# Optimization experiments

Measured on AMD Instinct MI355X. Metric: run time of the kernel, lower is better.

Reference implementation:

```python
import jax, jax.numpy as jnp
import numpy as np

EPS = 1e-6

def setup_inputs() -> dict:
    key = jax.random.key(0)
    k1, k2, k3 = jax.random.split(key, 3)
    D = 1024
    return {
        "x": jax.random.normal(k1, (2, 2048, D), dtype=jnp.float32),
        "w_norm": jnp.ones((D,), dtype=jnp.float32),
        "w_qkv": jax.random.normal(k2, (3 * D, D), dtype=jnp.float32) * (1.0 / np.sqrt(D)),
        "w_out": jax.random.normal(k3, (D, D), dtype=jnp.float32) * (1.0 / np.sqrt(D)),
        "window_size": 128,
        "n_heads": 16,
    }

def reference(x, w_norm, w_qkv, w_out, window_size, n_heads):
    B, L, D = x.shape
    H = n_heads
    dh = D // H
    skip = x
    # RMSNorm
    rms = jnp.sqrt(jnp.mean(x * x, axis=-1, keepdims=True) + EPS)
    xn = w_norm * (x / rms)
    # QKV projection (torch Linear: y = x @ W.T)
    qkv = xn @ w_qkv.T  # [B, L, 3D]
    q, k, v = jnp.split(qkv, 3, axis=-1)
    q = q.reshape(B, L, H, dh).transpose(0, 2, 1, 3)  # [B,H,L,dh]
    k = k.reshape(B, L, H, dh).transpose(0, 2, 1, 3)
    v = v.reshape(B, L, H, dh).transpose(0, 2, 1, 3)
    scores = jnp.einsum("bhid,bhjd->bhij", q, k) / np.sqrt(dh)  # [B,H,L,L]
    # Symmetric window: token i attends to j in [i - w//2, i + w//2]
    idx = jnp.arange(L)
    half = window_size // 2
    band = jnp.abs(idx[:, None] - idx[None, :]) <= half  # [L, L]
    scores = jnp.where(band, scores, -jnp.inf)
    attn = jax.nn.softmax(scores, axis=-1)  # zeros outside band, matches torch loop
    out = jnp.einsum("bhij,bhjd->bhid", attn, v)  # [B,H,L,dh]
    out = out.transpose(0, 2, 1, 3).reshape(B, L, D)
    out = out @ w_out.T
    return out + skip
```

## Files before the change

kernel.cpp:

```cpp
#include <hip/hip_runtime.h>
#include <hip/hip_bf16.h>
#include <cstdint>

typedef float f32x4 __attribute__((ext_vector_type(4)));
typedef short s16x8 __attribute__((ext_vector_type(8)));
typedef short s16x4 __attribute__((ext_vector_type(4)));

constexpr int B_ = 2, L_ = 2048, D_ = 1024, H_ = 16, DH = 64, HALF = 64;
constexpr int M_ROWS = B_ * L_;
constexpr int QKV_N = 3 * D_;

__device__ __forceinline__ void gload16(const void* g, void* l) {
    __builtin_amdgcn_global_load_lds(
        (const __attribute__((address_space(1))) unsigned int*)g,
        (__attribute__((address_space(3))) unsigned int*)l, 16, 0, 0);
}

__device__ __forceinline__ void cfence() {
    __builtin_amdgcn_sched_barrier(0);
    asm volatile("" ::: "memory");
}

__global__ __launch_bounds__(256) void rmsnorm_kernel(const float* __restrict__ x,
                                                      const float* __restrict__ wn,
                                                      __hip_bfloat16* __restrict__ xn) {
    int w = threadIdx.x >> 6, lane = threadIdx.x & 63;
    int row = blockIdx.x * 4 + w;
    const float4* xr = reinterpret_cast<const float4*>(x + (size_t)row * D_);
    const float4* wr = reinterpret_cast<const float4*>(wn);
    float4 v[4];
    float ss = 0.f;
#pragma unroll
    for (int c = 0; c < 4; ++c) {
        v[c] = xr[c * 64 + lane];
        ss += v[c].x * v[c].x + v[c].y * v[c].y + v[c].z * v[c].z + v[c].w * v[c].w;
    }
#pragma unroll
    for (int off = 32; off; off >>= 1) ss += __shfl_xor(ss, off);
    float rinv = rsqrtf(ss * (1.0f / D_) + 1e-6f);
#pragma unroll
    for (int c = 0; c < 4; ++c) {
        float4 wv = wr[c * 64 + lane];
        s16x4 pk;
        float vals[4] = {v[c].x * rinv * wv.x, v[c].y * rinv * wv.y,
                         v[c].z * rinv * wv.z, v[c].w * rinv * wv.w};
#pragma unroll
        for (int e = 0; e < 4; ++e) {
            __hip_bfloat16 t = __float2bfloat16(vals[e]);
            pk[e] = *reinterpret_cast<short*>(&t);
        }
        *(s16x4*)(xn + (size_t)row * D_ + (c * 64 + lane) * 4) = pk;
    }
}

__global__ void cvt_weights_kernel(const float* __restrict__ wq, const float* __restrict__ wo,
                                   __hip_bfloat16* __restrict__ oq, __hip_bfloat16* __restrict__ oo) {
    constexpr int NQ4 = QKV_N * D_ / 4;
    int i = blockIdx.x * blockDim.x + threadIdx.x;
    const float* src; __hip_bfloat16* dst; int j;
    if (i < NQ4) { src = wq; dst = oq; j = i; }
    else         { src = wo; dst = oo; j = i - NQ4; }
    float4 v = reinterpret_cast<const float4*>(src)[j];
    s16x4 pk;
    float vals[4] = {v.x, v.y, v.z, v.w};
#pragma unroll
    for (int e = 0; e < 4; ++e) {
        __hip_bfloat16 t = __float2bfloat16(vals[e]);
        pk[e] = *reinterpret_cast<short*>(&t);
    }
    *(s16x4*)(dst + (size_t)j * 4) = pk;
}

template <int EPI, int BN>
__global__ __launch_bounds__(256, 2) void gemm_pipe_kernel(const __hip_bfloat16* __restrict__ A,
                                                           const __hip_bfloat16* __restrict__ Bt,
                                                           __hip_bfloat16* __restrict__ Cbf,
                                                           __hip_bfloat16* __restrict__ vT,
                                                           float* __restrict__ Cf,
                                                           const float* __restrict__ resid,
                                                           int M, int N, int K) {
    constexpr int BM = 128;
    constexpr int NFR = BN / 32;
    constexpr int ABYTES = BM * 128;
    constexpr int BBYTES = BN * 128;
    constexpr int BUF = ABYTES + BBYTES;
    constexpr int AISS = BM / 32, BISS = BN / 32, NISS = AISS + BISS;
    __shared__ __align__(16) char smem[2 * BUF];

    const int tid = threadIdx.x;
    const int lane = tid & 63;
    const int wid = tid >> 6;

    int nwg = gridDim.x * gridDim.y;
    int lin = blockIdx.y * gridDim.x + blockIdx.x;
    int cpx = nwg >> 3;
    int swz = (lin & 7) * cpx + (lin >> 3);
    int bx = swz % gridDim.x;
    int by = swz / gridDim.x;

    const int rowBase = by * BM;
    const int colBase = bx * BN;
    const int NTILES = K >> 6;

    const int srow = tid >> 3;
    const int colSw = ((tid & 7) ^ (srow & 7)) << 3;
    const __hip_bfloat16* aG = A + (size_t)(rowBase + srow) * K + colSw;
    const __hip_bfloat16* bG = Bt + (size_t)(colBase + srow) * K + colSw;
    const int dstW = wid << 10;

    const int wm = wid >> 1, wn = wid & 1;
    const int l15 = lane & 15, hi = lane >> 4;
    const int s7 = l15 & 7;
    const int rA = wm * 64 + l15;
    const int rB = wn * (BN / 2) + l15;

    f32x4 acc[4][NFR];
#pragma unroll
    for (int m = 0; m < 4; ++m)
#pragma unroll
        for (int n = 0; n < NFR; ++n) acc[m][n] = (f32x4){0.f, 0.f, 0.f, 0.f};

#pragma unroll
    for (int i = 0; i < AISS; ++i) gload16(aG + (size_t)(i * 32) * K, smem + i * 4096 + dstW);
#pragma unroll
    for (int i = 0; i < BISS; ++i) gload16(bG + (size_t)(i * 32) * K, smem + ABYTES + i * 4096 + dstW);

    for (int kt = 0; kt < NTILES; ++kt) {
        const int bf = kt & 1;
        if (kt + 1 < NTILES) {
            char* base = smem + (bf ^ 1) * BUF;
            const __hip_bfloat16* as = aG + (size_t)(kt + 1) * 64;
            const __hip_bfloat16* bs = bG + (size_t)(kt + 1) * 64;
#pragma unroll
            for (int i = 0; i < AISS; ++i) gload16(as + (size_t)(i * 32) * K, base + i * 4096 + dstW);
#pragma unroll
            for (int i = 0; i < BISS; ++i) gload16(bs + (size_t)(i * 32) * K, base + ABYTES + i * 4096 + dstW);
            if constexpr (NISS == 8)
                asm volatile("s_waitcnt vmcnt(8)" ::: "memory");
            else
                asm volatile("s_waitcnt vmcnt(6)" ::: "memory");
        } else {
            asm volatile("s_waitcnt vmcnt(0)" ::: "memory");
        }
        __builtin_amdgcn_s_barrier();
        cfence();

        const char* ab = smem + bf * BUF;
        const char* bb = ab + ABYTES;
        s16x8 af[4][2], bfr[NFR][2];
#pragma unroll
        for (int mf = 0; mf < 4; ++mf)
#pragma unroll
            for (int kk = 0; kk < 2; ++kk)
                af[mf][kk] = *(const s16x8*)(ab + (rA + mf * 16) * 128 + (((kk * 4 + hi) ^ s7) << 4));
#pragma unroll
        for (int nf = 0; nf < NFR; ++nf)
#pragma unroll
            for (int kk = 0; kk < 2; ++kk)
                bfr[nf][kk] = *(const s16x8*)(bb + (rB + nf * 16) * 128 + (((kk * 4 + hi) ^ s7) << 4));

        __builtin_amdgcn_s_setprio(1);
#pragma unroll
        for (int kk = 0; kk < 2; ++kk)
#pragma unroll
            for (int mf = 0; mf < 4; ++mf)
#pragma unroll
                for (int nf = 0; nf < NFR; ++nf)
                    acc[mf][nf] = __builtin_amdgcn_mfma_f32_16x16x32_bf16(af[mf][kk], bfr[nf][kk],
                                                                          acc[mf][nf], 0, 0, 0);
        __builtin_amdgcn_s_setprio(0);

        asm volatile("s_waitcnt lgkmcnt(0)" ::: "memory");
        __builtin_amdgcn_s_barrier();
        cfence();
    }

    if constexpr (EPI == 0) {
        if (colBase < 2 * D_) {
#pragma unroll
            for (int mf = 0; mf < 4; ++mf)
#pragma unroll
                for (int nf = 0; nf < NFR; ++nf) {
                    int col = colBase + wn * (BN / 2) + nf * 16 + l15;
                    int row0 = rowBase + wm * 64 + mf * 16 + 4 * hi;
#pragma unroll
                    for (int r = 0; r < 4; ++r)
                        Cbf[(size_t)(row0 + r) * N + col] = __float2bfloat16(acc[mf][nf][r]);
                }
        } else {
            char* Ct = smem;
#pragma unroll
            for (int mf = 0; mf < 4; ++mf)
#pragma unroll
                for (int nf = 0; nf < NFR; ++nf) {
                    int cl = wn * (BN / 2) + nf * 16 + l15;
#pragma unroll
                    for (int r = 0; r < 4; ++r) {
                        int rl = wm * 64 + mf * 16 + 4 * hi + r;
                        __hip_bfloat16 t = __float2bfloat16(acc[mf][nf][r]);
                        *(short*)(Ct + cl * 272 + rl * 2) = *reinterpret_cast<short*>(&t);
                    }
                }
            __syncthreads();
            int cl = tid >> 1, half = tid & 1;
            int gcol = colBase + cl - 2 * D_;
            int hh = gcol >> 6, dd = gcol & 63;
            int bb2 = rowBase >> 11, i0 = rowBase & (L_ - 1);
            __hip_bfloat16* dstp = vT + ((size_t)(bb2 * H_ + hh) * DH + dd) * L_ + i0 + half * 64;
#pragma unroll
            for (int ch = 0; ch < 8; ++ch) {
                s16x8 vv = *(const s16x8*)(Ct + cl * 272 + half * 128 + ch * 16);
                *(s16x8*)(dstp + ch * 8) = vv;
            }
        }
    } else {
#pragma unroll
        for (int mf = 0; mf < 4; ++mf)
#pragma unroll
            for (int nf = 0; nf < NFR; ++nf) {
                int col = colBase + wn * (BN / 2) + nf * 16 + l15;
                int row0 = rowBase + wm * 64 + mf * 16 + 4 * hi;
#pragma unroll
                for (int r = 0; r < 4; ++r)
                    Cf[(size_t)(row0 + r) * N + col] = acc[mf][nf][r] + resid[(size_t)(row0 + r) * N + col];
            }
    }
}

__global__ __launch_bounds__(128) void attn_mfma_kernel(const __hip_bfloat16* __restrict__ qkv,
                                                        const __hip_bfloat16* __restrict__ vT,
                                                        __hip_bfloat16* __restrict__ attn) {
    __shared__ __align__(16) char smem[49152];
    constexpr int VOFF = 24576;
    int tid = threadIdx.x;
    int lane = tid & 63, w = tid >> 6;
    int tq = blockIdx.x, h = blockIdx.y, b = blockIdx.z;
    int q0 = tq * 64;
    int jg0 = q0 - HALF;
    const __hip_bfloat16* qkvb = qkv + (size_t)(b * L_) * QKV_N;
    const __hip_bfloat16* vTg = vT + (size_t)(b * H_ + h) * DH * L_;

    int l15 = lane & 15, hi = lane >> 4;

    s16x8 aq[2][2];
#pragma unroll
    for (int m = 0; m < 2; ++m)
#pragma unroll
        for (int kk = 0; kk < 2; ++kk)
            aq[m][kk] = *(const s16x8*)(qkvb + (size_t)(q0 + 32 * w + 16 * m + l15) * QKV_N
                                        + h * DH + kk * 32 + hi * 8);

#pragma unroll
    for (int it = 0; it < 12; ++it) {
        int ob = (it * 2 + w) << 10;
        int o = ob + lane * 16;
        int row = o >> 7;
        int c = ((o >> 4) & 7) ^ (row & 7);
        int jg = jg0 + row;
        int jc = jg < 0 ? 0 : (jg > L_ - 1 ? L_ - 1 : jg);
        gload16(qkvb + (size_t)jc * QKV_N + D_ + h * DH + c * 8, smem + ob);
    }
#pragma unroll
    for (int it = 0; it < 12; ++it) {
        int ob = (it * 2 + w) << 10;
        int o = ob + lane * 16;
        int d = o / 384;
        int rem = o - d * 384;
        int c = (rem >> 4) ^ (d & 7);
        int kb = jg0 + c * 8;
        int kc = kb < 0 ? 0 : (kb > L_ - 8 ? L_ - 8 : kb);
        gload16(vTg + (size_t)d * L_ + kc, smem + VOFF + ob);
    }
    asm volatile("s_waitcnt vmcnt(12)" ::: "memory");
    __builtin_amdgcn_s_barrier();
    cfence();

    f32x4 sc[2][10];
#pragma unroll
    for (int m = 0; m < 2; ++m)
#pragma unroll
        for (int kt = 0; kt < 10; ++kt) sc[m][kt] = (f32x4){0.f, 0.f, 0.f, 0.f};

#pragma unroll
    for (int kt = 0; kt < 10; ++kt) {
        int jl = 32 * w + 16 * kt + l15;
        s16x8 bk0 = *(const s16x8*)(smem + jl * 128 + ((hi ^ (jl & 7)) * 16));
        s16x8 bk1 = *(const s16x8*)(smem + jl * 128 + (((4 + hi) ^ (jl & 7)) * 16));
#pragma unroll
        for (int m = 0; m < 2; ++m) {
            sc[m][kt] = __builtin_amdgcn_mfma_f32_16x16x32_bf16(aq[m][0], bk0, sc[m][kt], 0, 0, 0);
            sc[m][kt] = __builtin_amdgcn_mfma_f32_16x16x32_bf16(aq[m][1], bk1, sc[m][kt], 0, 0, 0);
        }
    }

#pragma unroll
    for (int m = 0; m < 2; ++m) {
#pragma unroll
        for (int r = 0; r < 4; ++r) {
            int iloc = 32 * w + 16 * m + 4 * hi + r;
            float mx = -1e30f;
#pragma unroll
            for (int kt = 0; kt < 10; ++kt) {
                int jl = 32 * w + 16 * kt + l15;
                int jg = jg0 + jl;
                bool ok = (jl >= iloc) && (jl <= iloc + 2 * HALF) && (jg >= 0) && (jg < L_);
                float s = ok ? sc[m][kt][r] * 0.125f : -1e30f;
                sc[m][kt][r] = s;
                mx = fmaxf(mx, s);
            }
            mx = fmaxf(mx, __shfl_xor(mx, 1));
            mx = fmaxf(mx, __shfl_xor(mx, 2));
            mx = fmaxf(mx, __shfl_xor(mx, 4));
            mx = fmaxf(mx, __shfl_xor(mx, 8));
            float sum = 0.f;
#pragma unroll
            for (int kt = 0; kt < 10; ++kt) {
                float p = __expf(sc[m][kt][r] - mx);
                sc[m][kt][r] = p;
                sum += p;
            }
            sum += __shfl_xor(sum, 1);
            sum += __shfl_xor(sum, 2);
            sum += __shfl_xor(sum, 4);
            sum += __shfl_xor(sum, 8);
            float inv = 1.0f / sum;
#pragma unroll
            for (int kt = 0; kt < 10; ++kt) sc[m][kt][r] *= inv;
        }
    }

    __syncthreads();

    {
        __hip_bfloat16* Pw = (__hip_bfloat16*)(smem + w * 10752);
#pragma unroll
        for (int m = 0; m < 2; ++m)
#pragma unroll
            for (int kt = 0; kt < 10; ++kt)
#pragma unroll
                for (int r = 0; r < 4; ++r)
                    Pw[(16 * m + 4 * hi + r) * 168 + 16 * kt + l15] = __float2bfloat16(sc[m][kt][r]);
    }
    __syncthreads();

    f32x4 o[2][4];
#pragma unroll
    for (int m = 0; m < 2; ++m)
#pragma unroll
        for (int nt = 0; nt < 4; ++nt) o[m][nt] = (f32x4){0.f, 0.f, 0.f, 0.f};

#pragma unroll
    for (int kst = 0; kst < 5; ++kst) {
        s16x8 ap[2];
#pragma unroll
        for (int m = 0; m < 2; ++m)
            ap[m] = *(const s16x8*)(smem + w * 10752 + (16 * m + l15) * 336 + (32 * kst + 8 * hi) * 2);
#pragma unroll
        for (int nt = 0; nt < 4; ++nt) {
            int d = 16 * nt + l15;
            int c = 4 * w + 4 * kst + hi;
            s16x8 bv = *(const s16x8*)(smem + VOFF + d * 384 + ((c ^ (d & 7)) << 4));
#pragma unroll
            for (int m = 0; m < 2; ++m)
                o[m][nt] = __builtin_amdgcn_mfma_f32_16x16x32_bf16(ap[m], bv, o[m][nt], 0, 0, 0);
        }
    }

#pragma unroll
    for (int m = 0; m < 2; ++m)
#pragma unroll
        for (int nt = 0; nt < 4; ++nt)
#pragma unroll
            for (int r = 0; r < 4; ++r) {
                int rowg = q0 + 32 * w + 16 * m + 4 * hi + r;
                attn[(size_t)(b * L_ + rowg) * D_ + h * DH + 16 * nt + l15] =
                    __float2bfloat16(o[m][nt][r]);
            }
}

extern "C" void kernel_launch(void* const* d_in, const int* in_sizes, int n_in,
                              void* d_out, int out_size, void* d_ws, size_t ws_size,
                              hipStream_t stream) {
    const float* x      = (const float*)d_in[0];
    const float* w_norm = (const float*)d_in[1];
    const float* w_qkv  = (const float*)d_in[2];
    const float* w_out  = (const float*)d_in[3];

    char* ws = (char*)d_ws;
    __hip_bfloat16* xn   = (__hip_bfloat16*)(ws);
    __hip_bfloat16* wq   = (__hip_bfloat16*)(ws + (8u  << 20));
    __hip_bfloat16* wo   = (__hip_bfloat16*)(ws + (14u << 20));
    __hip_bfloat16* qkv  = (__hip_bfloat16*)(ws + (16u << 20));
    __hip_bfloat16* attn = (__hip_bfloat16*)(ws + (40u << 20));
    __hip_bfloat16* vT   = (__hip_bfloat16*)(ws + (48u << 20));
    float* out = (float*)d_out;

    {
        int n4 = (QKV_N * D_ + D_ * D_) / 4;
        cvt_weights_kernel<<<n4 / 256, 256, 0, stream>>>(w_qkv, w_out, wq, wo);
    }

    rmsnorm_kernel<<<M_ROWS / 4, 256, 0, stream>>>(x, w_norm, xn);

    gemm_pipe_kernel<0, 128><<<dim3(QKV_N / 128, M_ROWS / 128), 256, 0, stream>>>(
        xn, wq, qkv, vT, nullptr, nullptr, M_ROWS, QKV_N, D_);

    attn_mfma_kernel<<<dim3(L_ / 64, H_, B_), 128, 0, stream>>>(qkv, vT, attn);

    gemm_pipe_kernel<1, 64><<<dim3(D_ / 64, M_ROWS / 128), 256, 0, stream>>>(
        attn, wo, nullptr, nullptr, out, x, M_ROWS, D_, D_);
}
```

Before: 92.35 us.

## Rewrite windowed attention with 32x32 MFMA and register-resident softmax; merge prep kernels

The attention kernel is rewritten to compute transposed scores with 32x32x16 MFMA, loading K and V fragments straight from global memory instead of staging them in LDS. Softmax runs in registers with only cross-half shuffles. P is repacked to bf16 through permlane32_swap, so the LDS round trip and its barriers are gone, and normalization is deferred to the output. Separately, weight conversion and RMSNorm are merged into one launch to save a kernel launch. The risk is uncoalesced, redundant global loads of K/V per wave in exchange for occupancy and fewer syncs.

```diff
diff --git a/kernel.cpp b/kernel.cpp
--- a/kernel.cpp
+++ b/kernel.cpp
@@ -3,8 +3,11 @@
 #include <cstdint>
 
 typedef float f32x4 __attribute__((ext_vector_type(4)));
+typedef float f32x16 __attribute__((ext_vector_type(16)));
 typedef short s16x8 __attribute__((ext_vector_type(8)));
 typedef short s16x4 __attribute__((ext_vector_type(4)));
+typedef unsigned int u32x2 __attribute__((ext_vector_type(2)));
+typedef unsigned int u32x4 __attribute__((ext_vector_type(4)));
 
 constexpr int B_ = 2, L_ = 2048, D_ = 1024, H_ = 16, DH = 64, HALF = 64;
 constexpr int M_ROWS = B_ * L_;
@@ -21,54 +24,60 @@
     asm volatile("" ::: "memory");
 }
 
-__global__ __launch_bounds__(256) void rmsnorm_kernel(const float* __restrict__ x,
-                                                      const float* __restrict__ wn,
-                                                      __hip_bfloat16* __restrict__ xn) {
-    int w = threadIdx.x >> 6, lane = threadIdx.x & 63;
-    int row = blockIdx.x * 4 + w;
-    const float4* xr = reinterpret_cast<const float4*>(x + (size_t)row * D_);
-    const float4* wr = reinterpret_cast<const float4*>(wn);
-    float4 v[4];
-    float ss = 0.f;
-#pragma unroll
-    for (int c = 0; c < 4; ++c) {
-        v[c] = xr[c * 64 + lane];
-        ss += v[c].x * v[c].x + v[c].y * v[c].y + v[c].z * v[c].z + v[c].w * v[c].w;
-    }
-#pragma unroll
-    for (int off = 32; off; off >>= 1) ss += __shfl_xor(ss, off);
-    float rinv = rsqrtf(ss * (1.0f / D_) + 1e-6f);
-#pragma unroll
-    for (int c = 0; c < 4; ++c) {
-        float4 wv = wr[c * 64 + lane];
+__global__ __launch_bounds__(256) void prep_kernel(const float* __restrict__ x,
+                                                   const float* __restrict__ wn,
+                                                   const float* __restrict__ wq,
+                                                   const float* __restrict__ wo,
+                                                   __hip_bfloat16* __restrict__ xn,
+                                                   __hip_bfloat16* __restrict__ oq,
+                                                   __hip_bfloat16* __restrict__ oo) {
+    constexpr int NQ4 = QKV_N * D_ / 4;
+    constexpr int NCVT = NQ4 + D_ * D_ / 4;
+    constexpr int CVTBLK = NCVT / 256;
+    int bid = blockIdx.x;
+    if (bid < CVTBLK) {
+        int i = bid * 256 + threadIdx.x;
+        const float* src; __hip_bfloat16* dst; int j;
+        if (i < NQ4) { src = wq; dst = oq; j = i; }
+        else         { src = wo; dst = oo; j = i - NQ4; }
+        float4 v = reinterpret_cast<const float4*>(src)[j];
         s16x4 pk;
-        float vals[4] = {v[c].x * rinv * wv.x, v[c].y * rinv * wv.y,
-                         v[c].z * rinv * wv.z, v[c].w * rinv * wv.w};
+        float vals[4] = {v.x, v.y, v.z, v.w};
 #pragma unroll
         for (int e = 0; e < 4; ++e) {
             __hip_bfloat16 t = __float2bfloat16(vals[e]);
             pk[e] = *reinterpret_cast<short*>(&t);
         }
-        *(s16x4*)(xn + (size_t)row * D_ + (c * 64 + lane) * 4) = pk;
-    }
-}
-
-__global__ void cvt_weights_kernel(const float* __restrict__ wq, const float* __restrict__ wo,
-                                   __hip_bfloat16* __restrict__ oq, __hip_bfloat16* __restrict__ oo) {
-    constexpr int NQ4 = QKV_N * D_ / 4;
-    int i = blockIdx.x * blockDim.x + threadIdx.x;
-    const float* src; __hip_bfloat16* dst; int j;
-    if (i < NQ4) { src = wq; dst = oq; j = i; }
-    else         { src = wo; dst = oo; j = i - NQ4; }
-    float4 v = reinterpret_cast<const float4*>(src)[j];
-    s16x4 pk;
-    float vals[4] = {v.x, v.y, v.z, v.w};
-#pragma unroll
-    for (int e = 0; e < 4; ++e) {
-        __hip_bfloat16 t = __float2bfloat16(vals[e]);
-        pk[e] = *reinterpret_cast<short*>(&t);
-    }
-    *(s16x4*)(dst + (size_t)j * 4) = pk;
+        *(s16x4*)(dst + (size_t)j * 4) = pk;
+    } else {
+        int w = threadIdx.x >> 6, lane = threadIdx.x & 63;
+        int row = (bid - CVTBLK) * 4 + w;
+        const float4* xr = reinterpret_cast<const float4*>(x + (size_t)row * D_);
+        const float4* wr = reinterpret_cast<const float4*>(wn);
+        float4 v[4];
+        float ss = 0.f;
+#pragma unroll
+        for (int c = 0; c < 4; ++c) {
+            v[c] = xr[c * 64 + lane];
+            ss += v[c].x * v[c].x + v[c].y * v[c].y + v[c].z * v[c].z + v[c].w * v[c].w;
+        }
+#pragma unroll
+        for (int off = 32; off; off >>= 1) ss += __shfl_xor(ss, off);
+        float rinv = rsqrtf(ss * (1.0f / D_) + 1e-6f);
+#pragma unroll
+        for (int c = 0; c < 4; ++c) {
+            float4 wv = wr[c * 64 + lane];
+            s16x4 pk;
+            float vals[4] = {v[c].x * rinv * wv.x, v[c].y * rinv * wv.y,
+                             v[c].z * rinv * wv.z, v[c].w * rinv * wv.w};
+#pragma unroll
+            for (int e = 0; e < 4; ++e) {
+                __hip_bfloat16 t = __float2bfloat16(vals[e]);
+                pk[e] = *reinterpret_cast<short*>(&t);
+            }
+            *(s16x4*)(xn + (size_t)row * D_ + (c * 64 + lane) * 4) = pk;
+        }
+    }
 }
 
 template <int EPI, int BN>
@@ -227,155 +236,113 @@
     }
 }
 
-__global__ __launch_bounds__(128) void attn_mfma_kernel(const __hip_bfloat16* __restrict__ qkv,
-                                                        const __hip_bfloat16* __restrict__ vT,
-                                                        __hip_bfloat16* __restrict__ attn) {
-    __shared__ __align__(16) char smem[49152];
-    constexpr int VOFF = 24576;
+__global__ __launch_bounds__(128, 2) void attn_mfma_kernel(const __hip_bfloat16* __restrict__ qkv,
+                                                           const __hip_bfloat16* __restrict__ vT,
+                                                           __hip_bfloat16* __restrict__ attn) {
     int tid = threadIdx.x;
-    int lane = tid & 63, w = tid >> 6;
+    int w = tid >> 6;
+    int lane = tid & 63;
+    int l31 = lane & 31, hi1 = lane >> 5;
     int tq = blockIdx.x, h = blockIdx.y, b = blockIdx.z;
-    int q0 = tq * 64;
-    int jg0 = q0 - HALF;
+    int qbase = tq * 64 + 32 * w;
+    int kb = qbase - HALF;
+    int qg = qbase + l31;
     const __hip_bfloat16* qkvb = qkv + (size_t)(b * L_) * QKV_N;
     const __hip_bfloat16* vTg = vT + (size_t)(b * H_ + h) * DH * L_;
 
-    int l15 = lane & 15, hi = lane >> 4;
-
-    s16x8 aq[2][2];
-#pragma unroll
-    for (int m = 0; m < 2; ++m)
-#pragma unroll
-        for (int kk = 0; kk < 2; ++kk)
-            aq[m][kk] = *(const s16x8*)(qkvb + (size_t)(q0 + 32 * w + 16 * m + l15) * QKV_N
-                                        + h * DH + kk * 32 + hi * 8);
-
-#pragma unroll
-    for (int it = 0; it < 12; ++it) {
-        int ob = (it * 2 + w) << 10;
-        int o = ob + lane * 16;
-        int row = o >> 7;
-        int c = ((o >> 4) & 7) ^ (row & 7);
-        int jg = jg0 + row;
-        int jc = jg < 0 ? 0 : (jg > L_ - 1 ? L_ - 1 : jg);
-        gload16(qkvb + (size_t)jc * QKV_N + D_ + h * DH + c * 8, smem + ob);
-    }
-#pragma unroll
-    for (int it = 0; it < 12; ++it) {
-        int ob = (it * 2 + w) << 10;
-        int o = ob + lane * 16;
-        int d = o / 384;
-        int rem = o - d * 384;
-        int c = (rem >> 4) ^ (d & 7);
-        int kb = jg0 + c * 8;
-        int kc = kb < 0 ? 0 : (kb > L_ - 8 ? L_ - 8 : kb);
-        gload16(vTg + (size_t)d * L_ + kc, smem + VOFF + ob);
-    }
-    asm volatile("s_waitcnt vmcnt(12)" ::: "memory");
-    __builtin_amdgcn_s_barrier();
-    cfence();
-
-    f32x4 sc[2][10];
-#pragma unroll
-    for (int m = 0; m < 2; ++m)
-#pragma unroll
-        for (int kt = 0; kt < 10; ++kt) sc[m][kt] = (f32x4){0.f, 0.f, 0.f, 0.f};
-
-#pragma unroll
-    for (int kt = 0; kt < 10; ++kt) {
-        int jl = 32 * w + 16 * kt + l15;
-        s16x8 bk0 = *(const s16x8*)(smem + jl * 128 + ((hi ^ (jl & 7)) * 16));
-        s16x8 bk1 = *(const s16x8*)(smem + jl * 128 + (((4 + hi) ^ (jl & 7)) * 16));
-#pragma unroll
-        for (int m = 0; m < 2; ++m) {
-            sc[m][kt] = __builtin_amdgcn_mfma_f32_16x16x32_bf16(aq[m][0], bk0, sc[m][kt], 0, 0, 0);
-            sc[m][kt] = __builtin_amdgcn_mfma_f32_16x16x32_bf16(aq[m][1], bk1, sc[m][kt], 0, 0, 0);
-        }
-    }
-
-#pragma unroll
-    for (int m = 0; m < 2; ++m) {
-#pragma unroll
-        for (int r = 0; r < 4; ++r) {
-            int iloc = 32 * w + 16 * m + 4 * hi + r;
-            float mx = -1e30f;
-#pragma unroll
-            for (int kt = 0; kt < 10; ++kt) {
-                int jl = 32 * w + 16 * kt + l15;
-                int jg = jg0 + jl;
-                bool ok = (jl >= iloc) && (jl <= iloc + 2 * HALF) && (jg >= 0) && (jg < L_);
-                float s = ok ? sc[m][kt][r] * 0.125f : -1e30f;
-                sc[m][kt][r] = s;
-                mx = fmaxf(mx, s);
+    s16x8 qf[4];
+#pragma unroll
+    for (int kk = 0; kk < 4; ++kk)
+        qf[kk] = *(const s16x8*)(qkvb + (size_t)qg * QKV_N + h * DH + kk * 16 + hi1 * 8);
+
+    f32x16 T[5];
+#pragma unroll
+    for (int kt = 0; kt < 5; ++kt) T[kt] = (f32x16)(0.f);
+#pragma unroll
+    for (int kt = 0; kt < 5; ++kt) {
+        int keyg = kb + 32 * kt + l31;
+        int kc = keyg < 0 ? 0 : (keyg > L_ - 1 ? L_ - 1 : keyg);
+        const __hip_bfloat16* kp = qkvb + (size_t)kc * QKV_N + D_ + h * DH + hi1 * 8;
+#pragma unroll
+        for (int kk = 0; kk < 4; ++kk) {
+            s16x8 kf = *(const s16x8*)(kp + kk * 16);
+            T[kt] = __builtin_amdgcn_mfma_f32_32x32x16_bf16(kf, qf[kk], T[kt], 0, 0, 0);
+        }
+    }
+
+    float mx = -1e30f;
+#pragma unroll
+    for (int kt = 0; kt < 5; ++kt) {
+#pragma unroll
+        for (int r = 0; r < 16; ++r) {
+            int koff = (r & 3) + 8 * (r >> 2) + 4 * hi1;
+            int keyg = kb + 32 * kt + koff;
+            int del = keyg - qg;
+            bool ok = (del >= -HALF) && (del <= HALF) && (keyg >= 0) && (keyg < L_);
+            float t = ok ? T[kt][r] * 0.125f : -1e30f;
+            T[kt][r] = t;
+            mx = fmaxf(mx, t);
+        }
+    }
+    mx = fmaxf(mx, __shfl_xor(mx, 32));
+    float sum = 0.f;
+#pragma unroll
+    for (int kt = 0; kt < 5; ++kt) {
+#pragma unroll
+        for (int r = 0; r < 16; ++r) {
+            float p = __expf(T[kt][r] - mx);
+            T[kt][r] = p;
+            sum += p;
+        }
+    }
+    sum += __shfl_xor(sum, 32);
+    float inv = 1.0f / sum;
+
+    u32x4 pu[10];
+#pragma unroll
+    for (int kt = 0; kt < 5; ++kt) {
+#pragma unroll
+        for (int s = 0; s < 2; ++s) {
+            unsigned P0, P1, P2, P3;
+            asm("v_cvt_pk_bf16_f32 %0, %1, %2" : "=v"(P0) : "v"(T[kt][8 * s + 0]), "v"(T[kt][8 * s + 1]));
+            asm("v_cvt_pk_bf16_f32 %0, %1, %2" : "=v"(P1) : "v"(T[kt][8 * s + 2]), "v"(T[kt][8 * s + 3]));
+            asm("v_cvt_pk_bf16_f32 %0, %1, %2" : "=v"(P2) : "v"(T[kt][8 * s + 4]), "v"(T[kt][8 * s + 5]));
+            asm("v_cvt_pk_bf16_f32 %0, %1, %2" : "=v"(P3) : "v"(T[kt][8 * s + 6]), "v"(T[kt][8 * s + 7]));
+            u32x2 sA = __builtin_amdgcn_permlane32_swap(P0, P2, false, false);
+            u32x2 sB = __builtin_amdgcn_permlane32_swap(P1, P3, false, false);
+            pu[2 * kt + s] = (u32x4){sA[0], sB[0], sA[1], sB[1]};
+        }
+    }
+
+    f32x16 O[2];
+#pragma unroll
+    for (int dt = 0; dt < 2; ++dt) O[dt] = (f32x16)(0.f);
+#pragma unroll
+    for (int t = 0; t < 10; ++t) {
+        int kv = kb + 16 * t + 8 * hi1;
+        kv = kv < 0 ? 0 : (kv > L_ - 8 ? L_ - 8 : kv);
+        s16x8 pf = __builtin_bit_cast(s16x8, pu[t]);
+#pragma unroll
+        for (int dt = 0; dt < 2; ++dt) {
+            s16x8 vf = *(const s16x8*)(vTg + (size_t)(32 * dt + l31) * L_ + kv);
+            O[dt] = __builtin_amdgcn_mfma_f32_32x32x16_bf16(vf, pf, O[dt], 0, 0, 0);
+        }
+    }
+
+    __hip_bfloat16* ob = attn + (size_t)(b * L_ + qg) * D_ + h * DH;
+#pragma unroll
+    for (int dt = 0; dt < 2; ++dt) {
+#pragma unroll
+        for (int rr = 0; rr < 4; ++rr) {
+            s16x4 pk4;
+#pragma unroll
+            for (int j = 0; j < 4; ++j) {
+                __hip_bfloat16 tb = __float2bfloat16(O[dt][4 * rr + j] * inv);
+                pk4[j] = *reinterpret_cast<short*>(&tb);
             }
-            mx = fmaxf(mx, __shfl_xor(mx, 1));
-            mx = fmaxf(mx, __shfl_xor(mx, 2));
-            mx = fmaxf(mx, __shfl_xor(mx, 4));
-            mx = fmaxf(mx, __shfl_xor(mx, 8));
-            float sum = 0.f;
-#pragma unroll
-            for (int kt = 0; kt < 10; ++kt) {
-                float p = __expf(sc[m][kt][r] - mx);
-                sc[m][kt][r] = p;
-                sum += p;
-            }
-            sum += __shfl_xor(sum, 1);
-            sum += __shfl_xor(sum, 2);
-            sum += __shfl_xor(sum, 4);
-            sum += __shfl_xor(sum, 8);
-            float inv = 1.0f / sum;
-#pragma unroll
-            for (int kt = 0; kt < 10; ++kt) sc[m][kt][r] *= inv;
-        }
-    }
-
-    __syncthreads();
-
-    {
-        __hip_bfloat16* Pw = (__hip_bfloat16*)(smem + w * 10752);
-#pragma unroll
-        for (int m = 0; m < 2; ++m)
-#pragma unroll
-            for (int kt = 0; kt < 10; ++kt)
-#pragma unroll
-                for (int r = 0; r < 4; ++r)
-                    Pw[(16 * m + 4 * hi + r) * 168 + 16 * kt + l15] = __float2bfloat16(sc[m][kt][r]);
-    }
-    __syncthreads();
-
-    f32x4 o[2][4];
-#pragma unroll
-    for (int m = 0; m < 2; ++m)
-#pragma unroll
-        for (int nt = 0; nt < 4; ++nt) o[m][nt] = (f32x4){0.f, 0.f, 0.f, 0.f};
-
-#pragma unroll
-    for (int kst = 0; kst < 5; ++kst) {
-        s16x8 ap[2];
-#pragma unroll
-        for (int m = 0; m < 2; ++m)
-            ap[m] = *(const s16x8*)(smem + w * 10752 + (16 * m + l15) * 336 + (32 * kst + 8 * hi) * 2);
-#pragma unroll
-        for (int nt = 0; nt < 4; ++nt) {
-            int d = 16 * nt + l15;
-            int c = 4 * w + 4 * kst + hi;
-            s16x8 bv = *(const s16x8*)(smem + VOFF + d * 384 + ((c ^ (d & 7)) << 4));
-#pragma unroll
-            for (int m = 0; m < 2; ++m)
-                o[m][nt] = __builtin_amdgcn_mfma_f32_16x16x32_bf16(ap[m], bv, o[m][nt], 0, 0, 0);
-        }
-    }
-
-#pragma unroll
-    for (int m = 0; m < 2; ++m)
-#pragma unroll
-        for (int nt = 0; nt < 4; ++nt)
-#pragma unroll
-            for (int r = 0; r < 4; ++r) {
-                int rowg = q0 + 32 * w + 16 * m + 4 * hi + r;
-                attn[(size_t)(b * L_ + rowg) * D_ + h * DH + 16 * nt + l15] =
-                    __float2bfloat16(o[m][nt][r]);
-            }
+            *(s16x4*)(ob + 32 * dt + 8 * rr + 4 * hi1) = pk4;
+        }
+    }
 }
 
 extern "C" void kernel_launch(void* const* d_in, const int* in_sizes, int n_in,
@@ -395,12 +362,7 @@
     __hip_bfloat16* vT   = (__hip_bfloat16*)(ws + (48u << 20));
     float* out = (float*)d_out;
 
-    {
-        int n4 = (QKV_N * D_ + D_ * D_) / 4;
-        cvt_weights_kernel<<<n4 / 256, 256, 0, stream>>>(w_qkv, w_out, wq, wo);
-    }
-
-    rmsnorm_kernel<<<M_ROWS / 4, 256, 0, stream>>>(x, w_norm, xn);
+    prep_kernel<<<4096 + M_ROWS / 4, 256, 0, stream>>>(x, w_norm, w_qkv, w_out, xn, wq, wo);
 
     gemm_pipe_kernel<0, 128><<<dim3(QKV_N / 128, M_ROWS / 128), 256, 0, stream>>>(
         xn, wq, qkv, vT, nullptr, nullptr, M_ROWS, QKV_N, D_);
```

Measured after the change: 86.25 us. 6.6% less time.
